# Optimization experiments

Measured on AMD Instinct MI355X. Metric: run time of the kernel, lower is better.

Reference implementation:

```python
import jax, jax.numpy as jnp
import numpy as np

# DeepSpeed FixedSparsityConfig defaults (attention='unidirectional')
BLOCK = 16
NUM_LOCAL_BLOCKS = 4   # local window = 4 blocks = 64 tokens
D_MODEL = 1024
N_HEADS = 16
HEAD_DIM = D_MODEL // N_HEADS


def _block_layout(seq_len: int) -> np.ndarray:
    """Token-level boolean mask [S,S] from the fixed unidirectional block layout.
    Allowed iff: (same 4-block local window AND block_k <= block_q) OR
                 (block_k % 4 == 3 AND block_k <= block_q)  (causal global column).
    Same layout for every head (different_layout_per_head=False)."""
    nb = seq_len // BLOCK
    r = np.arange(nb)
    causal = r[None, :] <= r[:, None]
    same_win = (r[:, None] // NUM_LOCAL_BLOCKS) == (r[None, :] // NUM_LOCAL_BLOCKS)
    glob = (r[None, :] % NUM_LOCAL_BLOCKS) == (NUM_LOCAL_BLOCKS - 1)
    layout = (same_win & causal) | (glob & causal)
    return np.kron(layout, np.ones((BLOCK, BLOCK), dtype=bool))


def setup_inputs() -> dict:
    key = jax.random.key(0)
    ks = jax.random.split(key, 7)
    B, S = 2, 2048
    init = 1.0 / np.sqrt(D_MODEL)
    x = jax.random.normal(ks[0], (B, S, D_MODEL), jnp.float32)
    key_padding_mask = jnp.zeros((B, S), jnp.float32)  # additive mask ('add' mode)
    Wq = jax.random.normal(ks[1], (D_MODEL, D_MODEL), jnp.float32) * init
    Wk = jax.random.normal(ks[2], (D_MODEL, D_MODEL), jnp.float32) * init
    Wv = jax.random.normal(ks[3], (D_MODEL, D_MODEL), jnp.float32) * init
    bq = jax.random.normal(ks[4], (D_MODEL,), jnp.float32) * 0.01
    bk = jax.random.normal(ks[5], (D_MODEL,), jnp.float32) * 0.01
    bv = jax.random.normal(ks[6], (D_MODEL,), jnp.float32) * 0.01
    return dict(x=x, key_padding_mask=key_padding_mask,
                Wq=Wq, bq=bq, Wk=Wk, bk=bk, Wv=Wv, bv=bv)


def reference(x, key_padding_mask, Wq, bq, Wk, bk, Wv, bv):
    B, S, D = x.shape
    q = (x @ Wq + bq).reshape(B, S, N_HEADS, HEAD_DIM)
    k = (x @ Wk + bk).reshape(B, S, N_HEADS, HEAD_DIM)
    v = (x @ Wv + bv).reshape(B, S, N_HEADS, HEAD_DIM)
    scale = HEAD_DIM ** -0.5  # DeepSpeed scales by head_size**-0.5 inside softmax
    scores = jnp.einsum('bqhd,bkhd->bhqk', q, k) * scale
    scores = scores + key_padding_mask[:, None, None, :]
    mask = jnp.asarray(_block_layout(S))  # [S,S] bool; absent blocks excluded from softmax
    scores = jnp.where(mask[None, None], scores, -jnp.inf)
    attn = jax.nn.softmax(scores, axis=-1)
    out = jnp.einsum('bhqk,bkhd->bqhd', attn, v)
    return out.reshape(B, S, D)
```

## Files before the change

kernel.cpp:

```cpp
#include <hip/hip_runtime.h>
#include <hip/hip_bf16.h>

typedef __bf16 bf16;
typedef __bf16 bf16x4 __attribute__((ext_vector_type(4)));
typedef __bf16 bf16x8 __attribute__((ext_vector_type(8)));
typedef float  f32x4  __attribute__((ext_vector_type(4)));

#define D_MODEL 1024
#define S_LEN   2048
#define BATCH   2
#define NH      16
#define HD      64
#define NX ((size_t)BATCH * S_LEN * D_MODEL)

__device__ inline void gl_lds16(const bf16* g, bf16* l) {
    __builtin_amdgcn_global_load_lds(
        (const __attribute__((address_space(1))) void*)g,
        (__attribute__((address_space(3))) void*)l, 16, 0, 0);
}

__global__ __launch_bounds__(256) void cvt_x(
    const float* __restrict__ x, bf16* __restrict__ xb)
{
    const size_t base = ((size_t)blockIdx.x * 256 + threadIdx.x) * 8;
    const float4 a = *(const float4*)(x + base);
    const float4 b = *(const float4*)(x + base + 4);
    bf16x8 o;
    o[0] = (bf16)a.x; o[1] = (bf16)a.y; o[2] = (bf16)a.z; o[3] = (bf16)a.w;
    o[4] = (bf16)b.x; o[5] = (bf16)b.y; o[6] = (bf16)b.z; o[7] = (bf16)b.w;
    *(bf16x8*)(xb + base) = o;
}

__global__ __launch_bounds__(256) void wt_cvt(
    const float* __restrict__ Wq, const float* __restrict__ Wk,
    const float* __restrict__ Wv, bf16* __restrict__ Wt)
{
    const int z = blockIdx.z;
    const float* W = (z == 0) ? Wq : (z == 1) ? Wk : Wv;
    const int k0 = blockIdx.y * 64, n0 = blockIdx.x * 64;

    __shared__ bf16 tile[64 * 72];

    const int r16 = threadIdx.x >> 4, c4 = (threadIdx.x & 15) << 2;

#pragma unroll
    for (int rr = 0; rr < 4; ++rr) {
        const int row = rr * 16 + r16;
        const float4 v = *(const float4*)(W + (size_t)(k0 + row) * D_MODEL + n0 + c4);
        bf16x4 o; o[0] = (bf16)v.x; o[1] = (bf16)v.y; o[2] = (bf16)v.z; o[3] = (bf16)v.w;
        *(bf16x4*)(tile + row * 72 + c4) = o;
    }
    __syncthreads();
#pragma unroll
    for (int rr = 0; rr < 4; ++rr) {
        const int row = rr * 16 + r16;
        bf16x4 o;
#pragma unroll
        for (int j = 0; j < 4; ++j) o[j] = tile[(c4 + j) * 72 + row];
        *(bf16x4*)(Wt + (size_t)(z * D_MODEL + n0 + row) * D_MODEL + k0 + c4) = o;
    }
}

#define GNT 32

__device__ __forceinline__ void stage_tile(
    const bf16* __restrict__ Xb, const bf16* __restrict__ Wt,
    bf16* __restrict__ sA, bf16* __restrict__ sB,
    int m0, int n0, int k0, int tid, int wave)
{
    {
        const int ci0 = tid;
        const int r0 = ci0 >> 2, c0 = (ci0 & 3) ^ ((ci0 >> 3) & 3);
        gl_lds16(Xb + (size_t)(m0 + r0) * D_MODEL + k0 + c0 * 8, sA + wave * 512);
        const int ci1 = 512 + tid;
        const int r1 = ci1 >> 2, c1 = (ci1 & 3) ^ ((ci1 >> 3) & 3);
        gl_lds16(Xb + (size_t)(m0 + r1) * D_MODEL + k0 + c1 * 8, sA + 4096 + wave * 512);
    }
    {
        const int ci0 = tid;
        const int r0 = ci0 >> 2, c0 = (ci0 & 3) ^ ((ci0 >> 3) & 3);
        gl_lds16(Wt + (size_t)(n0 + r0) * D_MODEL + k0 + c0 * 8, sB + wave * 512);
        if (wave < 4) {
            const int ci1 = 512 + tid;
            const int r1 = ci1 >> 2, c1 = (ci1 & 3) ^ ((ci1 >> 3) & 3);
            gl_lds16(Wt + (size_t)(n0 + r1) * D_MODEL + k0 + c1 * 8, sB + 4096 + wave * 512);
        }
    }
}

template<int VM>
__device__ __forceinline__ void gemm_tile_body(
    const bf16* __restrict__ Xb, const bf16* __restrict__ Wt,
    bf16* __restrict__ As, bf16* __restrict__ Bs,
    int m0, int n0, int t, int tid, int wave, int wm, int wn,
    int col, int quad, int pchunk, f32x4 (&acc)[4][6])
{
    if constexpr (VM == 8)      asm volatile("s_waitcnt vmcnt(8)" ::: "memory");
    else if constexpr (VM == 4) asm volatile("s_waitcnt vmcnt(4)" ::: "memory");
    else                        asm volatile("s_waitcnt vmcnt(0)" ::: "memory");
    asm volatile("s_barrier" ::: "memory");

    const bf16* bufA = As + (t & 3) * 8192;
    const bf16* bufB = Bs + (t & 3) * 6144;

    bf16x8 a[4], b[6];
#pragma unroll
    for (int mr = 0; mr < 4; ++mr)
        a[mr] = *(const bf16x8*)(bufA + (wm * 64 + mr * 16 + col) * 32 + pchunk * 8);
#pragma unroll
    for (int nr = 0; nr < 6; ++nr)
        b[nr] = *(const bf16x8*)(bufB + (wn * 96 + nr * 16 + col) * 32 + pchunk * 8);

    if (t + 3 < GNT)
        stage_tile(Xb, Wt, As + ((t + 3) & 3) * 8192, Bs + ((t + 3) & 3) * 6144,
                   m0, n0, (t + 3) * 32, tid, wave);

    __builtin_amdgcn_s_setprio(1);
#pragma unroll
    for (int mr = 0; mr < 4; ++mr)
#pragma unroll
        for (int nr = 0; nr < 6; ++nr)
            acc[mr][nr] = __builtin_amdgcn_mfma_f32_16x16x32_bf16(a[mr], b[nr], acc[mr][nr], 0, 0, 0);
    __builtin_amdgcn_s_setprio(0);
}

__global__ __launch_bounds__(512, 2) void gemm_qkv_dp(
    const bf16* __restrict__ Xb, const bf16* __restrict__ Wt,
    const float* __restrict__ bq, const float* __restrict__ bk,
    const float* __restrict__ bv, bf16* __restrict__ QKV)
{
    extern __shared__ bf16 smem[];
    bf16* As = smem;
    bf16* Bs = smem + 32768;

    const int n0 = blockIdx.x * 192, m0 = blockIdx.y * 256;
    const int tid = threadIdx.x, wave = tid >> 6, lane = tid & 63;
    const int wm = wave >> 1, wn = wave & 1;
    const int col = lane & 15, quad = lane >> 4;
    const int pchunk = quad ^ ((col >> 1) & 3);

    f32x4 acc[4][6] = {};

    stage_tile(Xb, Wt, As,          Bs,          m0, n0,  0, tid, wave);
    stage_tile(Xb, Wt, As + 8192,   Bs + 6144,   m0, n0, 32, tid, wave);
    stage_tile(Xb, Wt, As + 16384,  Bs + 12288,  m0, n0, 64, tid, wave);

    for (int t = 0; t < GNT - 2; ++t)
        gemm_tile_body<8>(Xb, Wt, As, Bs, m0, n0, t, tid, wave, wm, wn, col, quad, pchunk, acc);
    gemm_tile_body<4>(Xb, Wt, As, Bs, m0, n0, GNT - 2, tid, wave, wm, wn, col, quad, pchunk, acc);
    gemm_tile_body<0>(Xb, Wt, As, Bs, m0, n0, GNT - 1, tid, wave, wm, wn, col, quad, pchunk, acc);

#pragma unroll
    for (int nr = 0; nr < 6; ++nr) {
        const int cg = n0 + wn * 96 + nr * 16 + col;
        const int z = cg >> 10, c = cg & 1023;
        const float bsv = (z == 0 ? bq : (z == 1 ? bk : bv))[c];
        const float scale = (z == 0) ? 0.125f : 1.0f;
        bf16* C = QKV + (size_t)z * NX;
#pragma unroll
        for (int mr = 0; mr < 4; ++mr)
#pragma unroll
            for (int i = 0; i < 4; ++i) {
                const int rg = m0 + wm * 64 + mr * 16 + quad * 4 + i;
                C[(size_t)rg * D_MODEL + c] = (bf16)((acc[mr][nr][i] + bsv) * scale);
            }
    }
}

__global__ __launch_bounds__(256) void sparse_attn64(
    const bf16* __restrict__ Q, const bf16* __restrict__ Kv,
    const bf16* __restrict__ Vv, const float* __restrict__ kpm,
    float* __restrict__ out)
{
    const int w = (gridDim.x - 1) - blockIdx.x;
    const int h = blockIdx.y, b = blockIdx.z;
    const int t = threadIdx.x, wavei = t >> 6, lane = t & 63;
    const int col = lane & 15, quad = lane >> 4;
    const int qb = 4 * w + wavei;

    __shared__ bf16 KbS[2][64 * 72];
    __shared__ bf16 VtS[2][64 * 72];
    __shared__ bf16 Ps[4][16 * 72];

    const size_t qrow = ((size_t)(b * S_LEN + qb * 16 + col)) * D_MODEL + h * HD;
    const bf16x8 aq0 = *(const bf16x8*)(Q + qrow + quad * 8);
    const bf16x8 aq1 = *(const bf16x8*)(Q + qrow + 32 + quad * 8);

    f32x4 o[4] = {};
    float lacc[4] = {0.f, 0.f, 0.f, 0.f};

    const int nGlob = (w + 3) >> 2;
    const int niter = nGlob + 1;

    const int srow = t >> 2, sd16 = (t & 3) << 4;
    const int sg = srow >> 4, sr = srow & 15;
    const int p2 = t & 31, dg8 = (t >> 5) << 3;
    const int key0 = 2 * p2, vg = key0 >> 4, vr = key0 & 15;

    auto kb_of = [&](int it, int g) -> int {
        if (it == nGlob) return 4 * w + g;
        const int j = 4 * it + g;
        return (j < w) ? (4 * j + 3) : 3;
    };

    bf16x8 rk0, rk1, rv0, rv1;
    {
        const size_t krow = ((size_t)(b * S_LEN + kb_of(0, sg) * 16 + sr)) * D_MODEL + h * HD + sd16;
        rk0 = *(const bf16x8*)(Kv + krow);
        rk1 = *(const bf16x8*)(Kv + krow + 8);
        const size_t vrow = ((size_t)(b * S_LEN + kb_of(0, vg) * 16 + vr)) * D_MODEL + h * HD + dg8;
        rv0 = *(const bf16x8*)(Vv + vrow);
        rv1 = *(const bf16x8*)(Vv + vrow + D_MODEL);
        *(bf16x8*)(KbS[0] + srow * 72 + sd16)     = rk0;
        *(bf16x8*)(KbS[0] + srow * 72 + sd16 + 8) = rk1;
#pragma unroll
        for (int j = 0; j < 8; ++j) {
            bf16 pr[2] = { rv0[j], rv1[j] };
            *(unsigned int*)(VtS[0] + (dg8 + j) * 72 + key0) = *(unsigned int*)pr;
        }
    }

    for (int it = 0; it < niter; ++it) {
        __syncthreads();
        const int cur = it & 1, nxt = cur ^ 1;
        const bool more = (it + 1 < niter);
        if (more) {
            const size_t krow = ((size_t)(b * S_LEN + kb_of(it + 1, sg) * 16 + sr)) * D_MODEL + h * HD + sd16;
            rk0 = *(const bf16x8*)(Kv + krow);
            rk1 = *(const bf16x8*)(Kv + krow + 8);
            const size_t vrow = ((size_t)(b * S_LEN + kb_of(it + 1, vg) * 16 + vr)) * D_MODEL + h * HD + dg8;
            rv0 = *(const bf16x8*)(Vv + vrow);
            rv1 = *(const bf16x8*)(Vv + vrow + D_MODEL);
        }

        const bf16* Kb = KbS[cur];
        const bf16* Vt = VtS[cur];

        f32x4 s[4];
        float mval[4];
        bool  val[4];
#pragma unroll
        for (int g = 0; g < 4; ++g) {
            int kb;
            if (it == nGlob) { kb = 4 * w + g; val[g] = (g <= wavei); }
            else { const int j = 4 * it + g; val[g] = (j < w); kb = val[g] ? (4 * j + 3) : 3; }
            mval[g] = kpm[b * S_LEN + kb * 16 + col];
            f32x4 z = {};
            const bf16x8 bk0 = *(const bf16x8*)(Kb + (g * 16 + col) * 72 + quad * 8);
            const bf16x8 bk1 = *(const bf16x8*)(Kb + (g * 16 + col) * 72 + 32 + quad * 8);
            z = __builtin_amdgcn_mfma_f32_16x16x32_bf16(aq0, bk0, z, 0, 0, 0);
            s[g] = __builtin_amdgcn_mfma_f32_16x16x32_bf16(aq1, bk1, z, 0, 0, 0);
        }

#pragma unroll
        for (int i = 0; i < 4; ++i) {
#pragma unroll
            for (int g = 0; g < 4; ++g) {
                const float si = val[g] ? (s[g][i] + mval[g]) : -1e30f;
                const float pv = __expf(si);
                lacc[i] += pv;
                Ps[wavei][(quad * 4 + i) * 72 + g * 16 + col] = (bf16)pv;
            }
        }

        const bf16x8 aP0 = *(const bf16x8*)(Ps[wavei] + col * 72 + quad * 8);
        const bf16x8 aP1 = *(const bf16x8*)(Ps[wavei] + col * 72 + 32 + quad * 8);
#pragma unroll
        for (int nt = 0; nt < 4; ++nt) {
            const bf16x8 b0 = *(const bf16x8*)(Vt + (nt * 16 + col) * 72 + quad * 8);
            const bf16x8 b1 = *(const bf16x8*)(Vt + (nt * 16 + col) * 72 + 32 + quad * 8);
            o[nt] = __builtin_amdgcn_mfma_f32_16x16x32_bf16(aP0, b0, o[nt], 0, 0, 0);
            o[nt] = __builtin_amdgcn_mfma_f32_16x16x32_bf16(aP1, b1, o[nt], 0, 0, 0);
        }

        if (more) {
            *(bf16x8*)(KbS[nxt] + srow * 72 + sd16)     = rk0;
            *(bf16x8*)(KbS[nxt] + srow * 72 + sd16 + 8) = rk1;
#pragma unroll
            for (int j = 0; j < 8; ++j) {
                bf16 pr[2] = { rv0[j], rv1[j] };
                *(unsigned int*)(VtS[nxt] + (dg8 + j) * 72 + key0) = *(unsigned int*)pr;
            }
        }
    }

#pragma unroll
    for (int i = 0; i < 4; ++i) {
        float rs = lacc[i];
        rs += __shfl_xor(rs, 1);
        rs += __shfl_xor(rs, 2);
        rs += __shfl_xor(rs, 4);
        rs += __shfl_xor(rs, 8);
        const float inv = 1.0f / rs;
        const int rg = b * S_LEN + qb * 16 + quad * 4 + i;
#pragma unroll
        for (int nt = 0; nt < 4; ++nt)
            out[(size_t)rg * D_MODEL + h * HD + nt * 16 + col] = o[nt][i] * inv;
    }
}

extern "C" void kernel_launch(void* const* d_in, const int* in_sizes, int n_in,
                              void* d_out, int out_size, void* d_ws, size_t ws_size,
                              hipStream_t stream)
{
    const float* x = nullptr; const float* kpm = nullptr;
    const float* Wp[3] = {nullptr, nullptr, nullptr};
    const float* bp[3] = {nullptr, nullptr, nullptr};
    int wn = 0, bn = 0;
    for (int i = 0; i < n_in; ++i) {
        const float* p = (const float*)d_in[i];
        const long s = in_sizes[i];
        if (s == (long)NX)            x = p;
        else if (s == BATCH * S_LEN)  kpm = p;
        else if (s == D_MODEL * D_MODEL && wn < 3) Wp[wn++] = p;
        else if (s == D_MODEL && bn < 3)           bp[bn++] = p;
    }

    bf16* Qb = (bf16*)d_ws;
    bf16* Kb = Qb + NX;
    bf16* Vb = Kb + NX;
    bf16* Xb = (bf16*)d_out;
    bf16* Wt = Xb + NX;
    float* outp = (float*)d_out;

    static bool attr_done = false;
    if (!attr_done) {
        (void)hipFuncSetAttribute(reinterpret_cast<const void*>(gemm_qkv_dp),
                                  hipFuncAttributeMaxDynamicSharedMemorySize, 114688);
        attr_done = true;
    }

    cvt_x<<<(int)(NX / 8 / 256), 256, 0, stream>>>(x, Xb);
    wt_cvt<<<dim3(16, 16, 3), 256, 0, stream>>>(Wp[0], Wp[1], Wp[2], Wt);

    gemm_qkv_dp<<<dim3(16, 16), 512, 114688, stream>>>(
        Xb, Wt, bp[0], bp[1], bp[2], Qb);

    sparse_attn64<<<dim3(S_LEN / 64, NH, BATCH), 256, 0, stream>>>(
        Qb, Kb, Vb, kpm, outp);
}
```

Baseline: 153.8 us.

## Fuse prep kernels, split GEMM B staging, remap block order, add MFMA priority

Merges the x conversion and weight transpose kernels into one launch to save a launch gap. The GEMM now stages A and B separately, splitting each k-step into two MFMA halves with a barrier between, so the B prefetch is issued mid-iteration, and the B second-half load is spread across all waves. GEMM and attention blocks are remapped to a grouped order meant to improve L2/XCD locality. Attention MFMAs get raised wave priority. The extra barrier per k-step adds sync cost, and the vmcnt wait counts may no longer match the new load distribution.

```diff
diff --git a/kernel.cpp b/kernel.cpp
--- a/kernel.cpp
+++ b/kernel.cpp
@@ -19,27 +19,28 @@
         (__attribute__((address_space(3))) void*)l, 16, 0, 0);
 }
 
-__global__ __launch_bounds__(256) void cvt_x(
-    const float* __restrict__ x, bf16* __restrict__ xb)
-{
-    const size_t base = ((size_t)blockIdx.x * 256 + threadIdx.x) * 8;
-    const float4 a = *(const float4*)(x + base);
-    const float4 b = *(const float4*)(x + base + 4);
-    bf16x8 o;
-    o[0] = (bf16)a.x; o[1] = (bf16)a.y; o[2] = (bf16)a.z; o[3] = (bf16)a.w;
-    o[4] = (bf16)b.x; o[5] = (bf16)b.y; o[6] = (bf16)b.z; o[7] = (bf16)b.w;
-    *(bf16x8*)(xb + base) = o;
-}
-
-__global__ __launch_bounds__(256) void wt_cvt(
+__global__ __launch_bounds__(256) void prep(
+    const float* __restrict__ x, bf16* __restrict__ xb,
     const float* __restrict__ Wq, const float* __restrict__ Wk,
     const float* __restrict__ Wv, bf16* __restrict__ Wt)
 {
-    const int z = blockIdx.z;
+    __shared__ bf16 tile[64 * 72];
+
+    if (blockIdx.x < 2048) {
+        const size_t base = ((size_t)blockIdx.x * 256 + threadIdx.x) * 8;
+        const float4 a = *(const float4*)(x + base);
+        const float4 b = *(const float4*)(x + base + 4);
+        bf16x8 o;
+        o[0] = (bf16)a.x; o[1] = (bf16)a.y; o[2] = (bf16)a.z; o[3] = (bf16)a.w;
+        o[4] = (bf16)b.x; o[5] = (bf16)b.y; o[6] = (bf16)b.z; o[7] = (bf16)b.w;
+        *(bf16x8*)(xb + base) = o;
+        return;
+    }
+
+    const int id2 = blockIdx.x - 2048;
+    const int z = id2 >> 8;
     const float* W = (z == 0) ? Wq : (z == 1) ? Wk : Wv;
-    const int k0 = blockIdx.y * 64, n0 = blockIdx.x * 64;
-
-    __shared__ bf16 tile[64 * 72];
+    const int k0 = ((id2 >> 4) & 15) * 64, n0 = (id2 & 15) * 64;
 
     const int r16 = threadIdx.x >> 4, c4 = (threadIdx.x & 15) << 2;
 
@@ -63,37 +64,37 @@
 
 #define GNT 32
 
-__device__ __forceinline__ void stage_tile(
-    const bf16* __restrict__ Xb, const bf16* __restrict__ Wt,
-    bf16* __restrict__ sA, bf16* __restrict__ sB,
-    int m0, int n0, int k0, int tid, int wave)
-{
-    {
-        const int ci0 = tid;
-        const int r0 = ci0 >> 2, c0 = (ci0 & 3) ^ ((ci0 >> 3) & 3);
-        gl_lds16(Xb + (size_t)(m0 + r0) * D_MODEL + k0 + c0 * 8, sA + wave * 512);
-        const int ci1 = 512 + tid;
-        const int r1 = ci1 >> 2, c1 = (ci1 & 3) ^ ((ci1 >> 3) & 3);
-        gl_lds16(Xb + (size_t)(m0 + r1) * D_MODEL + k0 + c1 * 8, sA + 4096 + wave * 512);
-    }
-    {
-        const int ci0 = tid;
-        const int r0 = ci0 >> 2, c0 = (ci0 & 3) ^ ((ci0 >> 3) & 3);
-        gl_lds16(Wt + (size_t)(n0 + r0) * D_MODEL + k0 + c0 * 8, sB + wave * 512);
-        if (wave < 4) {
-            const int ci1 = 512 + tid;
-            const int r1 = ci1 >> 2, c1 = (ci1 & 3) ^ ((ci1 >> 3) & 3);
-            gl_lds16(Wt + (size_t)(n0 + r1) * D_MODEL + k0 + c1 * 8, sB + 4096 + wave * 512);
-        }
-    }
+__device__ __forceinline__ void stage_A(
+    const bf16* __restrict__ Xb, bf16* __restrict__ sA,
+    int m0, int k0, int tid, int wave)
+{
+    const int ci0 = tid;
+    const int r0 = ci0 >> 2, c0 = (ci0 & 3) ^ ((ci0 >> 3) & 3);
+    gl_lds16(Xb + (size_t)(m0 + r0) * D_MODEL + k0 + c0 * 8, sA + wave * 512);
+    const int ci1 = 512 + tid;
+    const int r1 = ci1 >> 2, c1 = (ci1 & 3) ^ ((ci1 >> 3) & 3);
+    gl_lds16(Xb + (size_t)(m0 + r1) * D_MODEL + k0 + c1 * 8, sA + 4096 + wave * 512);
+}
+
+__device__ __forceinline__ void stage_B(
+    const bf16* __restrict__ Wt, bf16* __restrict__ sB,
+    int n0, int k0, int tid, int wave, int lane)
+{
+    const int ci0 = tid;
+    const int r0 = ci0 >> 2, c0 = (ci0 & 3) ^ ((ci0 >> 3) & 3);
+    gl_lds16(Wt + (size_t)(n0 + r0) * D_MODEL + k0 + c0 * 8, sB + wave * 512);
+    const int ci1 = 512 + wave * 32 + lane;
+    const int r1 = ci1 >> 2, c1 = (ci1 & 3) ^ ((ci1 >> 3) & 3);
+    if (lane < 32)
+        gl_lds16(Wt + (size_t)(n0 + r1) * D_MODEL + k0 + c1 * 8, sB + 4096 + wave * 256);
 }
 
 template<int VM>
 __device__ __forceinline__ void gemm_tile_body(
     const bf16* __restrict__ Xb, const bf16* __restrict__ Wt,
     bf16* __restrict__ As, bf16* __restrict__ Bs,
-    int m0, int n0, int t, int tid, int wave, int wm, int wn,
-    int col, int quad, int pchunk, f32x4 (&acc)[4][6])
+    int m0, int n0, int t, int tid, int wave, int lane, int wm, int wn,
+    int col, int pchunk, f32x4 (&acc)[4][6])
 {
     if constexpr (VM == 8)      asm volatile("s_waitcnt vmcnt(8)" ::: "memory");
     else if constexpr (VM == 4) asm volatile("s_waitcnt vmcnt(4)" ::: "memory");
@@ -102,24 +103,38 @@
 
     const bf16* bufA = As + (t & 3) * 8192;
     const bf16* bufB = Bs + (t & 3) * 6144;
+    const bool pf = (t + 3 < GNT);
+    const int k3 = (t + 3) * 32;
+
+    if (pf) stage_A(Xb, As + ((t + 3) & 3) * 8192, m0, k3, tid, wave);
 
     bf16x8 a[4], b[6];
 #pragma unroll
     for (int mr = 0; mr < 4; ++mr)
         a[mr] = *(const bf16x8*)(bufA + (wm * 64 + mr * 16 + col) * 32 + pchunk * 8);
 #pragma unroll
-    for (int nr = 0; nr < 6; ++nr)
+    for (int nr = 0; nr < 3; ++nr)
         b[nr] = *(const bf16x8*)(bufB + (wn * 96 + nr * 16 + col) * 32 + pchunk * 8);
 
-    if (t + 3 < GNT)
-        stage_tile(Xb, Wt, As + ((t + 3) & 3) * 8192, Bs + ((t + 3) & 3) * 6144,
-                   m0, n0, (t + 3) * 32, tid, wave);
-
     __builtin_amdgcn_s_setprio(1);
 #pragma unroll
     for (int mr = 0; mr < 4; ++mr)
 #pragma unroll
-        for (int nr = 0; nr < 6; ++nr)
+        for (int nr = 0; nr < 3; ++nr)
+            acc[mr][nr] = __builtin_amdgcn_mfma_f32_16x16x32_bf16(a[mr], b[nr], acc[mr][nr], 0, 0, 0);
+    __builtin_amdgcn_s_setprio(0);
+
+    asm volatile("s_barrier" ::: "memory");
+    if (pf) stage_B(Wt, Bs + ((t + 3) & 3) * 6144, n0, k3, tid, wave, lane);
+#pragma unroll
+    for (int nr = 3; nr < 6; ++nr)
+        b[nr] = *(const bf16x8*)(bufB + (wn * 96 + nr * 16 + col) * 32 + pchunk * 8);
+
+    __builtin_amdgcn_s_setprio(1);
+#pragma unroll
+    for (int mr = 0; mr < 4; ++mr)
+#pragma unroll
+        for (int nr = 3; nr < 6; ++nr)
             acc[mr][nr] = __builtin_amdgcn_mfma_f32_16x16x32_bf16(a[mr], b[nr], acc[mr][nr], 0, 0, 0);
     __builtin_amdgcn_s_setprio(0);
 }
@@ -133,7 +148,11 @@
     bf16* As = smem;
     bf16* Bs = smem + 32768;
 
-    const int n0 = blockIdx.x * 192, m0 = blockIdx.y * 256;
+    const int bid = blockIdx.x, k = bid & 7, j = bid >> 3;
+    const int nx = ((k >> 2) << 3) + (j & 7);
+    const int my = ((k & 3) << 2) + (j >> 3);
+    const int n0 = nx * 192, m0 = my * 256;
+
     const int tid = threadIdx.x, wave = tid >> 6, lane = tid & 63;
     const int wm = wave >> 1, wn = wave & 1;
     const int col = lane & 15, quad = lane >> 4;
@@ -141,14 +160,14 @@
 
     f32x4 acc[4][6] = {};
 
-    stage_tile(Xb, Wt, As,          Bs,          m0, n0,  0, tid, wave);
-    stage_tile(Xb, Wt, As + 8192,   Bs + 6144,   m0, n0, 32, tid, wave);
-    stage_tile(Xb, Wt, As + 16384,  Bs + 12288,  m0, n0, 64, tid, wave);
+    stage_A(Xb, As,         m0,  0, tid, wave);  stage_B(Wt, Bs,         n0,  0, tid, wave, lane);
+    stage_A(Xb, As + 8192,  m0, 32, tid, wave);  stage_B(Wt, Bs + 6144,  n0, 32, tid, wave, lane);
+    stage_A(Xb, As + 16384, m0, 64, tid, wave);  stage_B(Wt, Bs + 12288, n0, 64, tid, wave, lane);
 
     for (int t = 0; t < GNT - 2; ++t)
-        gemm_tile_body<8>(Xb, Wt, As, Bs, m0, n0, t, tid, wave, wm, wn, col, quad, pchunk, acc);
-    gemm_tile_body<4>(Xb, Wt, As, Bs, m0, n0, GNT - 2, tid, wave, wm, wn, col, quad, pchunk, acc);
-    gemm_tile_body<0>(Xb, Wt, As, Bs, m0, n0, GNT - 1, tid, wave, wm, wn, col, quad, pchunk, acc);
+        gemm_tile_body<8>(Xb, Wt, As, Bs, m0, n0, t, tid, wave, lane, wm, wn, col, pchunk, acc);
+    gemm_tile_body<4>(Xb, Wt, As, Bs, m0, n0, GNT - 2, tid, wave, lane, wm, wn, col, pchunk, acc);
+    gemm_tile_body<0>(Xb, Wt, As, Bs, m0, n0, GNT - 1, tid, wave, lane, wm, wn, col, pchunk, acc);
 
 #pragma unroll
     for (int nr = 0; nr < 6; ++nr) {
@@ -172,8 +191,12 @@
     const bf16* __restrict__ Vv, const float* __restrict__ kpm,
     float* __restrict__ out)
 {
-    const int w = (gridDim.x - 1) - blockIdx.x;
-    const int h = blockIdx.y, b = blockIdx.z;
+    const int lid = blockIdx.x + 32 * (blockIdx.y + 16 * blockIdx.z);
+    const int xk = lid & 7, j = lid >> 3;
+    const int pair = xk * 4 + (j & 3);
+    const int h = pair & 15, b = pair >> 4;
+    const int w = 31 - (j >> 2);
+
     const int t = threadIdx.x, wavei = t >> 6, lane = t & 63;
     const int col = lane & 15, quad = lane >> 4;
     const int qb = 4 * w + wavei;
@@ -199,8 +222,8 @@
 
     auto kb_of = [&](int it, int g) -> int {
         if (it == nGlob) return 4 * w + g;
-        const int j = 4 * it + g;
-        return (j < w) ? (4 * j + 3) : 3;
+        const int jj = 4 * it + g;
+        return (jj < w) ? (4 * jj + 3) : 3;
     };
 
     bf16x8 rk0, rk1, rv0, rv1;
@@ -214,9 +237,9 @@
         *(bf16x8*)(KbS[0] + srow * 72 + sd16)     = rk0;
         *(bf16x8*)(KbS[0] + srow * 72 + sd16 + 8) = rk1;
 #pragma unroll
-        for (int j = 0; j < 8; ++j) {
-            bf16 pr[2] = { rv0[j], rv1[j] };
-            *(unsigned int*)(VtS[0] + (dg8 + j) * 72 + key0) = *(unsigned int*)pr;
+        for (int jj = 0; jj < 8; ++jj) {
+            bf16 pr[2] = { rv0[jj], rv1[jj] };
+            *(unsigned int*)(VtS[0] + (dg8 + jj) * 72 + key0) = *(unsigned int*)pr;
         }
     }
 
@@ -243,13 +266,15 @@
         for (int g = 0; g < 4; ++g) {
             int kb;
             if (it == nGlob) { kb = 4 * w + g; val[g] = (g <= wavei); }
-            else { const int j = 4 * it + g; val[g] = (j < w); kb = val[g] ? (4 * j + 3) : 3; }
+            else { const int jj = 4 * it + g; val[g] = (jj < w); kb = val[g] ? (4 * jj + 3) : 3; }
             mval[g] = kpm[b * S_LEN + kb * 16 + col];
             f32x4 z = {};
             const bf16x8 bk0 = *(const bf16x8*)(Kb + (g * 16 + col) * 72 + quad * 8);
             const bf16x8 bk1 = *(const bf16x8*)(Kb + (g * 16 + col) * 72 + 32 + quad * 8);
+            __builtin_amdgcn_s_setprio(1);
             z = __builtin_amdgcn_mfma_f32_16x16x32_bf16(aq0, bk0, z, 0, 0, 0);
             s[g] = __builtin_amdgcn_mfma_f32_16x16x32_bf16(aq1, bk1, z, 0, 0, 0);
+            __builtin_amdgcn_s_setprio(0);
         }
 
 #pragma unroll
@@ -265,6 +290,7 @@
 
         const bf16x8 aP0 = *(const bf16x8*)(Ps[wavei] + col * 72 + quad * 8);
         const bf16x8 aP1 = *(const bf16x8*)(Ps[wavei] + col * 72 + 32 + quad * 8);
+        __builtin_amdgcn_s_setprio(1);
 #pragma unroll
         for (int nt = 0; nt < 4; ++nt) {
             const bf16x8 b0 = *(const bf16x8*)(Vt + (nt * 16 + col) * 72 + quad * 8);
@@ -272,14 +298,15 @@
             o[nt] = __builtin_amdgcn_mfma_f32_16x16x32_bf16(aP0, b0, o[nt], 0, 0, 0);
             o[nt] = __builtin_amdgcn_mfma_f32_16x16x32_bf16(aP1, b1, o[nt], 0, 0, 0);
         }
+        __builtin_amdgcn_s_setprio(0);
 
         if (more) {
             *(bf16x8*)(KbS[nxt] + srow * 72 + sd16)     = rk0;
             *(bf16x8*)(KbS[nxt] + srow * 72 + sd16 + 8) = rk1;
 #pragma unroll
-            for (int j = 0; j < 8; ++j) {
-                bf16 pr[2] = { rv0[j], rv1[j] };
-                *(unsigned int*)(VtS[nxt] + (dg8 + j) * 72 + key0) = *(unsigned int*)pr;
+            for (int jj = 0; jj < 8; ++jj) {
+                bf16 pr[2] = { rv0[jj], rv1[jj] };
+                *(unsigned int*)(VtS[nxt] + (dg8 + jj) * 72 + key0) = *(unsigned int*)pr;
             }
         }
     }
@@ -330,10 +357,9 @@
         attr_done = true;
     }
 
-    cvt_x<<<(int)(NX / 8 / 256), 256, 0, stream>>>(x, Xb);
-    wt_cvt<<<dim3(16, 16, 3), 256, 0, stream>>>(Wp[0], Wp[1], Wp[2], Wt);
-
-    gemm_qkv_dp<<<dim3(16, 16), 512, 114688, stream>>>(
+    prep<<<2816, 256, 0, stream>>>(x, Xb, Wp[0], Wp[1], Wp[2], Wt);
+
+    gemm_qkv_dp<<<dim3(256), 512, 114688, stream>>>(
         Xb, Wt, bp[0], bp[1], bp[2], Qb);
 
     sparse_attn64<<<dim3(S_LEN / 64, NH, BATCH), 256, 0, stream>>>(
```

Result: faster. 140.0 us (-8.9%).
